# Kernel optimization log

Hardware: AMD Instinct MI355X
Metric: run time of the kernel (lower is better)

Reference implementation:

```python
import jax, jax.numpy as jnp
from jax import lax
import numpy as np

DIM = 160
SHIFT_SIZE = 5
PAD = SHIFT_SIZE // 2
EPS = 1e-5


def conv1x1(x, w, b):
    # x: (B,C,D,H,W), w: (O,C), b: (O,)
    y = jnp.einsum('bcdhw,oc->bodhw', x, w)
    return y + b[None, :, None, None, None]


def groupnorm1(x, gamma, beta):
    # GroupNorm(1, C): normalize over (C,D,H,W) per sample, per-channel affine
    mu = jnp.mean(x, axis=(1, 2, 3, 4), keepdims=True)
    var = jnp.mean(jnp.square(x - mu), axis=(1, 2, 3, 4), keepdims=True)
    xhat = (x - mu) * lax.rsqrt(var + EPS)
    return xhat * gamma[None, :, None, None, None] + beta[None, :, None, None, None]


def axial_shift(x, axis):
    # pad -> channel-chunk -> per-chunk roll along `axis` -> cat -> narrow
    size = x.shape[axis]
    pad_width = [(0, 0)] * 5
    pad_width[axis] = (PAD, PAD)
    xp = jnp.pad(x, pad_width)
    chunks = jnp.split(xp, SHIFT_SIZE, axis=1)
    shifted = [jnp.roll(c, s, axis=axis)
               for c, s in zip(chunks, range(-PAD, PAD + 1))]
    xc = jnp.concatenate(shifted, axis=1)
    return lax.slice_in_dim(xc, PAD, PAD + size, axis=axis)


def setup_inputs() -> dict:
    key = jax.random.key(0)
    ks = jax.random.split(key, 16)
    B, C, D, H, W = 1, DIM, 48, 48, 48
    s = 0.05
    return {
        'x': jax.random.normal(ks[0], (B, C, D, H, W), jnp.float32),
        'w1': jax.random.normal(ks[1], (C, C), jnp.float32) * s,
        'b1': jnp.zeros((C,), jnp.float32),
        'g1': jnp.ones((C,), jnp.float32),
        'be1': jnp.zeros((C,), jnp.float32),
        'w21': jax.random.normal(ks[2], (C, C), jnp.float32) * s,
        'b21': jnp.zeros((C,), jnp.float32),
        'w22': jax.random.normal(ks[3], (C, C), jnp.float32) * s,
        'b22': jnp.zeros((C,), jnp.float32),
        'w23': jax.random.normal(ks[4], (C, C), jnp.float32) * s,
        'b23': jnp.zeros((C,), jnp.float32),
        'g2': jnp.ones((C,), jnp.float32),
        'be2': jnp.zeros((C,), jnp.float32),
        'w3': jax.random.normal(ks[5], (C, C), jnp.float32) * s,
        'b3': jnp.zeros((C,), jnp.float32),
    }


def reference(x, w1, b1, g1, be1, w21, b21, w22, b22, w23, b23, g2, be2, w3, b3):
    gelu = lambda t: jax.nn.gelu(t, approximate=False)  # torch nn.GELU default (erf)
    h = conv1x1(x, w1, b1)
    h = groupnorm1(h, g1, be1)
    h = gelu(h)
    x_lr = axial_shift(h, 2)  # torch_shift(x, shift_size, 2)
    x_td = axial_shift(h, 3)
    x_dp = axial_shift(h, 4)
    x_lr = gelu(conv1x1(x_lr, w21, b21))
    x_td = gelu(conv1x1(x_td, w22, b22))
    x_dp = gelu(conv1x1(x_dp, w23, b23))
    h = x_lr + x_td + x_dp
    h = groupnorm1(h, g2, be2)
    return conv1x1(h, w3, b3)
```

## Files before the change

kernel.cpp:

```cpp
#include <hip/hip_runtime.h>

#define SPATIAL 110592
#define CH 160
#define CPAD 168
#define NTOT (CH*SPATIAL)
#define WELEM (CH*CPAD)
#define W8 (WELEM/8)
#define NTILE 256
#define NBLK (SPATIAL/NTILE)
#define EPSV 1e-5f


typedef __attribute__((ext_vector_type(8))) short short8;
typedef __attribute__((ext_vector_type(4))) float f32x4;

#define MFMA(a,b,c) __builtin_amdgcn_mfma_f32_16x16x32_bf16((a),(b),(c),0,0,0)

__device__ __forceinline__ ushort f2bf(float f){
    union { float f; unsigned u; } v; v.f = f;
    return (ushort)((v.u + 0x7FFFu + ((v.u >> 16) & 1u)) >> 16);
}
__device__ __forceinline__ float gelu_f(float v){
    return 0.5f*v*(1.0f + erff(v*0.70710678118654752f));
}

__device__ __forceinline__ void block_reduce2_atomic8(float v0, float v1,
                                                      float* d0, float* d1){
    #pragma unroll
    for (int off = 32; off > 0; off >>= 1){
        v0 += __shfl_down(v0, off);
        v1 += __shfl_down(v1, off);
    }
    __shared__ float s0[8], s1[8];
    int wv = threadIdx.x >> 6, lane = threadIdx.x & 63;
    if (lane == 0){ s0[wv] = v0; s1[wv] = v1; }
    __syncthreads();
    if (threadIdx.x == 0){
        float a = 0.f, b = 0.f;
        #pragma unroll
        for (int i = 0; i < 8; ++i){ a += s0[i]; b += s1[i]; }
        atomicAdd(d0, a);
        atomicAdd(d1, b);
    }
}

__global__ __launch_bounds__(256)
void prep_weights(const float* __restrict__ w0, const float* __restrict__ w1,
                  const float* __restrict__ w2, const float* __restrict__ w3,
                  ushort* __restrict__ o0, ushort* __restrict__ o1,
                  ushort* __restrict__ o2, ushort* __restrict__ o3){
    const float* src[4] = {w0,w1,w2,w3};
    ushort*      dst[4] = {o0,o1,o2,o3};
    int m = blockIdx.y;
    int e = blockIdx.x*256 + threadIdx.x;
    if (e >= WELEM) return;
    int o = e / CPAD, c = e - o*CPAD;
    dst[m][e] = (c < CH) ? f2bf(src[m][o*CH + c]) : (ushort)0;
}

__global__ __launch_bounds__(512, 2)
void conv1_mfma(const float* __restrict__ x, const ushort* __restrict__ wp,
                const float* __restrict__ bias, float* __restrict__ h1c,
                float* __restrict__ stats){
    __shared__ ushort WL[CH][CPAD];
    int t = threadIdx.x;
    for (int k = t; k < W8; k += 512) ((short8*)WL)[k] = ((const short8*)wp)[k];
    __syncthreads();

    int v = (blockIdx.x & 7)*54 + (blockIdx.x >> 3);
    int s_base = v*NTILE;
    int l = t & 63, wv = t >> 6, ln = l & 15, lg = l >> 4;

    float lsum = 0.f, lsq = 0.f;

    #pragma unroll 1
    for (int ms = 0; ms < 2; ++ms){
        int sA = s_base + wv*32 + ms*16 + ln;

        short8 a[5];
        #pragma unroll
        for (int ks = 0; ks < 5; ++ks){
            const float* xp = x + (ks*32 + lg*8)*SPATIAL + sA;
            #pragma unroll
            for (int i = 0; i < 8; ++i)
                a[ks][i] = (short)f2bf(xp[i*SPATIAL]);
        }

        f32x4 acc[10];
        #pragma unroll
        for (int nt = 0; nt < 10; ++nt) acc[nt] = (f32x4)0.f;

        #pragma unroll
        for (int ks = 0; ks < 5; ++ks)
            #pragma unroll
            for (int nt = 0; nt < 10; ++nt){
                short8 b = *(const short8*)&WL[nt*16 + ln][ks*32 + lg*8];
                acc[nt] = MFMA(a[ks], b, acc[nt]);
            }

        #pragma unroll
        for (int nt = 0; nt < 10; ++nt){
            float bv = bias[nt*16 + ln];
            int kc = nt >> 1, ci = (nt & 1)*16 + ln;
            #pragma unroll
            for (int r = 0; r < 4; ++r){
                int srow = s_base + wv*32 + ms*16 + lg*4 + r;
                float val = acc[nt][r] + bv;
                h1c[(kc*SPATIAL + srow)*32 + ci] = val;
                lsum += val; lsq += val*val;
            }
        }
    }
    block_reduce2_atomic8(lsum, lsq, stats, stats+1);
}

__global__ __launch_bounds__(256)
void gn_gelu(const float* __restrict__ h, const float* __restrict__ g,
             const float* __restrict__ be, const float* __restrict__ stats,
             ushort* __restrict__ out){
    const float inv_n = 1.0f/(float)NTOT;
    float mu  = stats[0]*inv_n;
    float var = stats[1]*inv_n - mu*mu;
    float rs  = rsqrtf(var + EPSV);
    int nvec = NTOT/4;
    for (int i = blockIdx.x*256 + threadIdx.x; i < nvec; i += gridDim.x*256){
        int kc = (i >> 3) / SPATIAL;
        int c0 = kc*32 + (i & 7)*4;
        float4 gv = *(const float4*)&g[c0];
        float4 bv = *(const float4*)&be[c0];
        float4 x4 = ((const float4*)h)[i];
        ushort4 o;
        o.x = f2bf(gelu_f(fmaf(x4.x, rs*gv.x, bv.x - mu*rs*gv.x)));
        o.y = f2bf(gelu_f(fmaf(x4.y, rs*gv.y, bv.y - mu*rs*gv.y)));
        o.z = f2bf(gelu_f(fmaf(x4.z, rs*gv.z, bv.z - mu*rs*gv.z)));
        o.w = f2bf(gelu_f(fmaf(x4.w, rs*gv.w, bv.w - mu*rs*gv.w)));
        ((ushort4*)out)[i] = o;
    }
}

__global__ __launch_bounds__(512, 2)
void shift_conv3_mfma(const ushort* __restrict__ A2,
                      const ushort* __restrict__ w21p, const float* __restrict__ b21,
                      const ushort* __restrict__ w22p, const float* __restrict__ b22,
                      const ushort* __restrict__ w23p, const float* __restrict__ b23,
                      ushort* __restrict__ h2c, float* __restrict__ stats){
    __shared__ ushort WL[CH][CPAD];
    int t = threadIdx.x;
    int v = (blockIdx.x & 7)*54 + (blockIdx.x >> 3);
    int s_base = v*NTILE;
    int l = t & 63, wv = t >> 6, ln = l & 15, lg = l >> 4;

    float lsum = 0.f, lsq = 0.f;

    #pragma unroll 1
    for (int ms = 0; ms < 2; ++ms){
        int srow = s_base + wv*32 + ms*16 + ln;
        int d   = srow / 2304;
        int rem = srow - d*2304;
        int hh  = rem / 48;
        int ww  = rem - hh*48;

        f32x4 sum[10];
        #pragma unroll
        for (int nt = 0; nt < 10; ++nt) sum[nt] = (f32x4)0.f;

        #pragma unroll 1
        for (int br = 0; br < 3; ++br){
            const ushort* wp = (br == 0) ? w21p : (br == 1) ? w22p : w23p;
            const float*  bb = (br == 0) ? b21  : (br == 1) ? b22  : b23;
            int AS  = (br == 0) ? 2304 : (br == 1) ? 48 : 1;
            int crd = (br == 0) ? d    : (br == 1) ? hh : ww;

            __syncthreads();
            for (int k = t; k < W8; k += 512)
                ((short8*)WL)[k] = ((const short8*)wp)[k];
            __syncthreads();

            short8 a[5];
            #pragma unroll
            for (int ks = 0; ks < 5; ++ks){
                int sh = ks - 2;
                bool ok = ((unsigned)(crd - sh) < 48u);
                const short8* ap = (const short8*)
                    &A2[(ks*SPATIAL + srow - sh*AS)*32 + lg*8];
                short8 av = (short8)0;
                if (ok) av = *ap;
                a[ks] = av;
            }

            f32x4 acc[10];
            #pragma unroll
            for (int nt = 0; nt < 10; ++nt) acc[nt] = (f32x4)0.f;

            #pragma unroll
            for (int ks = 0; ks < 5; ++ks)
                #pragma unroll
                for (int nt = 0; nt < 10; ++nt){
                    short8 b = *(const short8*)&WL[nt*16 + ln][ks*32 + lg*8];
                    acc[nt] = MFMA(a[ks], b, acc[nt]);
                }

            #pragma unroll
            for (int nt = 0; nt < 10; ++nt){
                float bv = bb[nt*16 + ln];
                #pragma unroll
                for (int r = 0; r < 4; ++r)
                    sum[nt][r] += gelu_f(acc[nt][r] + bv);
            }
        }

        #pragma unroll
        for (int nt = 0; nt < 10; ++nt){
            int kc = nt >> 1, ci = (nt & 1)*16 + ln;
            #pragma unroll
            for (int r = 0; r < 4; ++r){
                int sr = s_base + wv*32 + ms*16 + lg*4 + r;
                float val = sum[nt][r];
                h2c[(kc*SPATIAL + sr)*32 + ci] = f2bf(val);
                lsum += val; lsq += val*val;
            }
        }
    }
    block_reduce2_atomic8(lsum, lsq, stats+2, stats+3);
}

__global__ void fold_conv3(const float* __restrict__ w3, const float* __restrict__ b3,
                           const float* __restrict__ g2, const float* __restrict__ be2,
                           const float* __restrict__ stats,
                           ushort* __restrict__ w3p, float* __restrict__ b3p){
    __shared__ float a_sh[CH], d_sh[CH];
    const float inv_n = 1.0f/(float)NTOT;
    float mu  = stats[2]*inv_n;
    float var = stats[3]*inv_n - mu*mu;
    float rs  = rsqrtf(var + EPSV);
    for (int c = threadIdx.x; c < CH; c += blockDim.x){
        float a = rs*g2[c];
        a_sh[c] = a;
        d_sh[c] = be2[c] - mu*a;
    }
    __syncthreads();
    for (int e = threadIdx.x; e < WELEM; e += blockDim.x){
        int o = e / CPAD, c = e - o*CPAD;
        w3p[e] = (c < CH) ? f2bf(w3[o*CH + c]*a_sh[c]) : (ushort)0;
    }
    for (int o = threadIdx.x; o < CH; o += blockDim.x){
        float acc = b3[o];
        for (int c = 0; c < CH; ++c) acc += w3[o*CH + c]*d_sh[c];
        b3p[o] = acc;
    }
}

__global__ __launch_bounds__(512, 2)
void conv3_mfma(const ushort* __restrict__ Xc, const ushort* __restrict__ wp,
                const float* __restrict__ bias, float* __restrict__ out){
    __shared__ ushort WL[CH][CPAD];
    int t = threadIdx.x;
    for (int k = t; k < W8; k += 512) ((short8*)WL)[k] = ((const short8*)wp)[k];
    __syncthreads();

    int v = (blockIdx.x & 7)*54 + (blockIdx.x >> 3);
    int s_base = v*NTILE;
    int l = t & 63, wv = t >> 6, ln = l & 15, lg = l >> 4;
    int sB0 = s_base + wv*32 + ln;

    f32x4 acc[10][2];
    #pragma unroll
    for (int mt = 0; mt < 10; ++mt){ acc[mt][0] = (f32x4)0.f; acc[mt][1] = (f32x4)0.f; }

    #pragma unroll
    for (int ks = 0; ks < 5; ++ks){
        short8 b[2];
        #pragma unroll
        for (int ns = 0; ns < 2; ++ns)
            b[ns] = *(const short8*)&Xc[(ks*SPATIAL + sB0 + ns*16)*32 + lg*8];
        #pragma unroll
        for (int mt = 0; mt < 10; ++mt){
            short8 a = *(const short8*)&WL[mt*16 + ln][ks*32 + lg*8];
            acc[mt][0] = MFMA(a, b[0], acc[mt][0]);
            acc[mt][1] = MFMA(a, b[1], acc[mt][1]);
        }
    }

    #pragma unroll
    for (int mt = 0; mt < 10; ++mt)
        #pragma unroll
        for (int r = 0; r < 4; ++r){
            float bv = bias[mt*16 + lg*4 + r];
            #pragma unroll
            for (int ns = 0; ns < 2; ++ns)
                out[(mt*16 + lg*4 + r)*SPATIAL + sB0 + ns*16] = acc[mt][ns][r] + bv;
        }
}

extern "C" void kernel_launch(void* const* d_in, const int* in_sizes, int n_in,
                              void* d_out, int out_size, void* d_ws, size_t ws_size,
                              hipStream_t stream){
    const float* x   = (const float*)d_in[0];
    const float* w1  = (const float*)d_in[1];
    const float* b1  = (const float*)d_in[2];
    const float* g1  = (const float*)d_in[3];
    const float* be1 = (const float*)d_in[4];
    const float* w21 = (const float*)d_in[5];
    const float* b21 = (const float*)d_in[6];
    const float* w22 = (const float*)d_in[7];
    const float* b22 = (const float*)d_in[8];
    const float* w23 = (const float*)d_in[9];
    const float* b23 = (const float*)d_in[10];
    const float* g2  = (const float*)d_in[11];
    const float* be2 = (const float*)d_in[12];
    const float* w3  = (const float*)d_in[13];
    const float* b3  = (const float*)d_in[14];

    float*  h1c   = (float*)d_ws;
    ushort* A2    = (ushort*)(h1c + NTOT);
    float*  stats = (float*)(A2 + NTOT);
    ushort* w1p   = (ushort*)(stats + 8);
    ushort* w21p  = w1p  + WELEM;
    ushort* w22p  = w21p + WELEM;
    ushort* w23p  = w22p + WELEM;
    ushort* w3p   = w23p + WELEM;
    float*  b3p   = (float*)(w3p + WELEM);
    ushort* h2c   = (ushort*)h1c;

    hipMemsetAsync(stats, 0, 4*sizeof(float), stream);

    prep_weights<<<dim3(WELEM/256, 4), dim3(256), 0, stream>>>(
        w1, w21, w22, w23, w1p, w21p, w22p, w23p);
    conv1_mfma<<<dim3(NBLK), dim3(512), 0, stream>>>(x, w1p, b1, h1c, stats);
    gn_gelu<<<dim3(2048), dim3(256), 0, stream>>>(h1c, g1, be1, stats, A2);
    shift_conv3_mfma<<<dim3(NBLK), dim3(512), 0, stream>>>(
        A2, w21p, b21, w22p, b22, w23p, b23, h2c, stats);
    fold_conv3<<<dim3(1), dim3(256), 0, stream>>>(w3, b3, g2, be2, stats, w3p, b3p);
    conv3_mfma<<<dim3(NBLK), dim3(512), 0, stream>>>(h2c, w3p, b3p, (float*)d_out);
}
```

Before: 396.9 us.

## Split output channels across blocks in all three MFMA conv kernels

Each conv kernel now handles a slice of output channels per block (2 slices for conv1, 5 for the shift conv and conv3), so the grid grows from 432 blocks to 864 or 2160. Shared-memory weight tiles shrink and the shift conv loads all three branch weight slices once, dropping its per-branch reload barriers. Occupancy hints rise to 8 blocks per CU. The aim is more parallelism and occupancy; the cost is that input activations (and in conv1 the fp32-to-bf16 conversion) are re-read or redone once per channel slice.

```diff
diff --git a/kernel.cpp b/kernel.cpp
--- a/kernel.cpp
+++ b/kernel.cpp
@@ -5,9 +5,6 @@
 #define CPAD 168
 #define NTOT (CH*SPATIAL)
 #define WELEM (CH*CPAD)
-#define W8 (WELEM/8)
-#define NTILE 256
-#define NBLK (SPATIAL/NTILE)
 #define EPSV 1e-5f
 
 
@@ -58,19 +55,22 @@
     dst[m][e] = (c < CH) ? f2bf(src[m][o*CH + c]) : (ushort)0;
 }
 
-__global__ __launch_bounds__(512, 2)
+__global__ __launch_bounds__(512, 8)
 void conv1_mfma(const float* __restrict__ x, const ushort* __restrict__ wp,
                 const float* __restrict__ bias, float* __restrict__ h1c,
                 float* __restrict__ stats){
-    __shared__ ushort WL[CH][CPAD];
+    __shared__ ushort WL[80][CPAD];
     int t = threadIdx.x;
-    for (int k = t; k < W8; k += 512) ((short8*)WL)[k] = ((const short8*)wp)[k];
-    __syncthreads();
-
-    int v = (blockIdx.x & 7)*54 + (blockIdx.x >> 3);
-    int s_base = v*NTILE;
+    int xcd = blockIdx.x & 7, r = blockIdx.x >> 3;
+    int osl = r & 1, sl = r >> 1;
+    int s_base = (xcd*54 + sl)*256;
+    int o_base = osl*80;
+
+    const short8* ws = (const short8*)(wp + o_base*CPAD);
+    for (int k = t; k < 80*CPAD/8; k += 512) ((short8*)WL)[k] = ws[k];
+    __syncthreads();
+
     int l = t & 63, wv = t >> 6, ln = l & 15, lg = l >> 4;
-
     float lsum = 0.f, lsq = 0.f;
 
     #pragma unroll 1
@@ -86,26 +86,27 @@
                 a[ks][i] = (short)f2bf(xp[i*SPATIAL]);
         }
 
-        f32x4 acc[10];
-        #pragma unroll
-        for (int nt = 0; nt < 10; ++nt) acc[nt] = (f32x4)0.f;
+        f32x4 acc[5];
+        #pragma unroll
+        for (int nt = 0; nt < 5; ++nt) acc[nt] = (f32x4)0.f;
 
         #pragma unroll
         for (int ks = 0; ks < 5; ++ks)
             #pragma unroll
-            for (int nt = 0; nt < 10; ++nt){
+            for (int nt = 0; nt < 5; ++nt){
                 short8 b = *(const short8*)&WL[nt*16 + ln][ks*32 + lg*8];
                 acc[nt] = MFMA(a[ks], b, acc[nt]);
             }
 
         #pragma unroll
-        for (int nt = 0; nt < 10; ++nt){
-            float bv = bias[nt*16 + ln];
-            int kc = nt >> 1, ci = (nt & 1)*16 + ln;
-            #pragma unroll
-            for (int r = 0; r < 4; ++r){
-                int srow = s_base + wv*32 + ms*16 + lg*4 + r;
-                float val = acc[nt][r] + bv;
+        for (int nt = 0; nt < 5; ++nt){
+            int oc = o_base + nt*16 + ln;
+            float bv = bias[oc];
+            int kc = oc >> 5, ci = oc & 31;
+            #pragma unroll
+            for (int q = 0; q < 4; ++q){
+                int srow = s_base + wv*32 + ms*16 + lg*4 + q;
+                float val = acc[nt][q] + bv;
                 h1c[(kc*SPATIAL + srow)*32 + ci] = val;
                 lsum += val; lsq += val*val;
             }
@@ -138,18 +139,29 @@
     }
 }
 
-__global__ __launch_bounds__(512, 2)
+__global__ __launch_bounds__(512, 8)
 void shift_conv3_mfma(const ushort* __restrict__ A2,
                       const ushort* __restrict__ w21p, const float* __restrict__ b21,
                       const ushort* __restrict__ w22p, const float* __restrict__ b22,
                       const ushort* __restrict__ w23p, const float* __restrict__ b23,
                       ushort* __restrict__ h2c, float* __restrict__ stats){
-    __shared__ ushort WL[CH][CPAD];
+    __shared__ ushort WL[3][32][CPAD];
     int t = threadIdx.x;
-    int v = (blockIdx.x & 7)*54 + (blockIdx.x >> 3);
-    int s_base = v*NTILE;
+    int xcd = blockIdx.x & 7, r = blockIdx.x >> 3;
+    int osl = r % 5, sl = r / 5;
+    int s_base = (xcd*54 + sl)*256;
+    int o_base = osl*32;
+
+    short8* wl8 = (short8*)WL;
+    const short8* w1s = (const short8*)(w21p + o_base*CPAD);
+    const short8* w2s = (const short8*)(w22p + o_base*CPAD);
+    const short8* w3s = (const short8*)(w23p + o_base*CPAD);
+    for (int k = t; k < 672; k += 512) wl8[k]        = w1s[k];
+    for (int k = t; k < 672; k += 512) wl8[672 + k]  = w2s[k];
+    for (int k = t; k < 672; k += 512) wl8[1344 + k] = w3s[k];
+    __syncthreads();
+
     int l = t & 63, wv = t >> 6, ln = l & 15, lg = l >> 4;
-
     float lsum = 0.f, lsq = 0.f;
 
     #pragma unroll 1
@@ -160,21 +172,14 @@
         int hh  = rem / 48;
         int ww  = rem - hh*48;
 
-        f32x4 sum[10];
-        #pragma unroll
-        for (int nt = 0; nt < 10; ++nt) sum[nt] = (f32x4)0.f;
+        f32x4 sum[2];
+        sum[0] = (f32x4)0.f; sum[1] = (f32x4)0.f;
 
         #pragma unroll 1
         for (int br = 0; br < 3; ++br){
-            const ushort* wp = (br == 0) ? w21p : (br == 1) ? w22p : w23p;
-            const float*  bb = (br == 0) ? b21  : (br == 1) ? b22  : b23;
+            const float* bb = (br == 0) ? b21 : (br == 1) ? b22 : b23;
             int AS  = (br == 0) ? 2304 : (br == 1) ? 48 : 1;
             int crd = (br == 0) ? d    : (br == 1) ? hh : ww;
-
-            __syncthreads();
-            for (int k = t; k < W8; k += 512)
-                ((short8*)WL)[k] = ((const short8*)wp)[k];
-            __syncthreads();
 
             short8 a[5];
             #pragma unroll
@@ -188,34 +193,34 @@
                 a[ks] = av;
             }
 
-            f32x4 acc[10];
-            #pragma unroll
-            for (int nt = 0; nt < 10; ++nt) acc[nt] = (f32x4)0.f;
+            f32x4 acc[2];
+            acc[0] = (f32x4)0.f; acc[1] = (f32x4)0.f;
 
             #pragma unroll
             for (int ks = 0; ks < 5; ++ks)
                 #pragma unroll
-                for (int nt = 0; nt < 10; ++nt){
-                    short8 b = *(const short8*)&WL[nt*16 + ln][ks*32 + lg*8];
+                for (int nt = 0; nt < 2; ++nt){
+                    short8 b = *(const short8*)&WL[br][nt*16 + ln][ks*32 + lg*8];
                     acc[nt] = MFMA(a[ks], b, acc[nt]);
                 }
 
             #pragma unroll
-            for (int nt = 0; nt < 10; ++nt){
-                float bv = bb[nt*16 + ln];
+            for (int nt = 0; nt < 2; ++nt){
+                float bv = bb[o_base + nt*16 + ln];
                 #pragma unroll
-                for (int r = 0; r < 4; ++r)
-                    sum[nt][r] += gelu_f(acc[nt][r] + bv);
-            }
-        }
-
-        #pragma unroll
-        for (int nt = 0; nt < 10; ++nt){
-            int kc = nt >> 1, ci = (nt & 1)*16 + ln;
-            #pragma unroll
-            for (int r = 0; r < 4; ++r){
-                int sr = s_base + wv*32 + ms*16 + lg*4 + r;
-                float val = sum[nt][r];
+                for (int q = 0; q < 4; ++q)
+                    sum[nt][q] += gelu_f(acc[nt][q] + bv);
+            }
+        }
+
+        #pragma unroll
+        for (int nt = 0; nt < 2; ++nt){
+            int oc = o_base + nt*16 + ln;
+            int kc = oc >> 5, ci = oc & 31;
+            #pragma unroll
+            for (int q = 0; q < 4; ++q){
+                int sr = s_base + wv*32 + ms*16 + lg*4 + q;
+                float val = sum[nt][q];
                 h2c[(kc*SPATIAL + sr)*32 + ci] = f2bf(val);
                 lsum += val; lsq += val*val;
             }
@@ -250,22 +255,26 @@
     }
 }
 
-__global__ __launch_bounds__(512, 2)
+__global__ __launch_bounds__(512, 8)
 void conv3_mfma(const ushort* __restrict__ Xc, const ushort* __restrict__ wp,
                 const float* __restrict__ bias, float* __restrict__ out){
-    __shared__ ushort WL[CH][CPAD];
+    __shared__ ushort WL[32][CPAD];
     int t = threadIdx.x;
-    for (int k = t; k < W8; k += 512) ((short8*)WL)[k] = ((const short8*)wp)[k];
-    __syncthreads();
-
-    int v = (blockIdx.x & 7)*54 + (blockIdx.x >> 3);
-    int s_base = v*NTILE;
+    int xcd = blockIdx.x & 7, r = blockIdx.x >> 3;
+    int osl = r % 5, sl = r / 5;
+    int s_base = (xcd*54 + sl)*256;
+    int o_base = osl*32;
+
+    const short8* ws = (const short8*)(wp + o_base*CPAD);
+    for (int k = t; k < 672; k += 512) ((short8*)WL)[k] = ws[k];
+    __syncthreads();
+
     int l = t & 63, wv = t >> 6, ln = l & 15, lg = l >> 4;
     int sB0 = s_base + wv*32 + ln;
 
-    f32x4 acc[10][2];
-    #pragma unroll
-    for (int mt = 0; mt < 10; ++mt){ acc[mt][0] = (f32x4)0.f; acc[mt][1] = (f32x4)0.f; }
+    f32x4 acc[2][2];
+    acc[0][0] = (f32x4)0.f; acc[0][1] = (f32x4)0.f;
+    acc[1][0] = (f32x4)0.f; acc[1][1] = (f32x4)0.f;
 
     #pragma unroll
     for (int ks = 0; ks < 5; ++ks){
@@ -274,7 +283,7 @@
         for (int ns = 0; ns < 2; ++ns)
             b[ns] = *(const short8*)&Xc[(ks*SPATIAL + sB0 + ns*16)*32 + lg*8];
         #pragma unroll
-        for (int mt = 0; mt < 10; ++mt){
+        for (int mt = 0; mt < 2; ++mt){
             short8 a = *(const short8*)&WL[mt*16 + ln][ks*32 + lg*8];
             acc[mt][0] = MFMA(a, b[0], acc[mt][0]);
             acc[mt][1] = MFMA(a, b[1], acc[mt][1]);
@@ -282,13 +291,14 @@
     }
 
     #pragma unroll
-    for (int mt = 0; mt < 10; ++mt)
-        #pragma unroll
-        for (int r = 0; r < 4; ++r){
-            float bv = bias[mt*16 + lg*4 + r];
+    for (int mt = 0; mt < 2; ++mt)
+        #pragma unroll
+        for (int q = 0; q < 4; ++q){
+            int o = o_base + mt*16 + lg*4 + q;
+            float bv = bias[o];
             #pragma unroll
             for (int ns = 0; ns < 2; ++ns)
-                out[(mt*16 + lg*4 + r)*SPATIAL + sB0 + ns*16] = acc[mt][ns][r] + bv;
+                out[o*SPATIAL + sB0 + ns*16] = acc[mt][ns][q] + bv;
         }
 }
 
@@ -324,12 +334,12 @@
 
     hipMemsetAsync(stats, 0, 4*sizeof(float), stream);
 
-    prep_weights<<<dim3(WELEM/256, 4), dim3(256), 0, stream>>>(
+    prep_weights<<<dim3((WELEM+255)/256, 4), dim3(256), 0, stream>>>(
         w1, w21, w22, w23, w1p, w21p, w22p, w23p);
-    conv1_mfma<<<dim3(NBLK), dim3(512), 0, stream>>>(x, w1p, b1, h1c, stats);
+    conv1_mfma<<<dim3(864), dim3(512), 0, stream>>>(x, w1p, b1, h1c, stats);
     gn_gelu<<<dim3(2048), dim3(256), 0, stream>>>(h1c, g1, be1, stats, A2);
-    shift_conv3_mfma<<<dim3(NBLK), dim3(512), 0, stream>>>(
+    shift_conv3_mfma<<<dim3(2160), dim3(512), 0, stream>>>(
         A2, w21p, b21, w22p, b22, w23p, b23, h2c, stats);
     fold_conv3<<<dim3(1), dim3(256), 0, stream>>>(w3, b3, g2, be2, stats, w3p, b3p);
-    conv3_mfma<<<dim3(NBLK), dim3(512), 0, stream>>>(h2c, w3p, b3p, (float*)d_out);
-}
+    conv3_mfma<<<dim3(2160), dim3(512), 0, stream>>>(h2c, w3p, b3p, (float*)d_out);
+}
```

Result: slower. 477.2 us (+20.2%).
